# Kernel tuning notes

Measured on AMD Instinct MI355X. Metric: run time of the kernel, lower is better.

Reference implementation:

```python
import jax, jax.numpy as jnp
import numpy as np

N = 2048; C_IN = 2; H = 32; EMB = 16; OUT = 1; HORIZON = 12
B = 32; T = 16

def setup_inputs() -> dict:
    key = jax.random.key(0)
    ks = jax.random.split(key, 10)
    s = 0.05
    return {
        "x":  jax.random.normal(ks[0], (B, T, N, C_IN), dtype=jnp.float32),
        "E1": jax.random.normal(ks[1], (N, EMB), dtype=jnp.float32) * 0.1,
        "E2": jax.random.normal(ks[2], (N, EMB), dtype=jnp.float32) * 0.1,
        "Wx": jax.random.normal(ks[3], (C_IN, 4 * H), dtype=jnp.float32) * s,
        "bx": jnp.zeros((4 * H,), dtype=jnp.float32),
        "Wh": jax.random.normal(ks[4], (H, 4 * H), dtype=jnp.float32) * s,
        "bh": jnp.zeros((4 * H,), dtype=jnp.float32),
        "Wp": jax.random.normal(ks[5], (H, OUT * HORIZON), dtype=jnp.float32) * s,
        "bp": jnp.zeros((OUT * HORIZON,), dtype=jnp.float32),
    }

def reference(x, E1, E2, Wx, bx, Wh, bh, Wp, bp):
    Bb, Tt, Nn, _ = x.shape
    # adaptive adjacency: softmax(relu(E1 @ E2^T)) over last dim  [N,N]
    A = jax.nn.softmax(jax.nn.relu(E1 @ E2.T), axis=-1)

    def step(carry, xt):
        h, c = carry  # [B,N,H]
        # fused graph-conv gates: (A @ xt) Wx + (A @ h) Wh + biases -> [B,N,4H]
        gates = (jnp.einsum('ij,bjc->bic', A, xt) @ Wx + bx
                 + jnp.einsum('ij,bjh->bih', A, h) @ Wh + bh)
        i, f, o, g = jnp.split(gates, 4, axis=-1)
        i = jax.nn.sigmoid(i); f = jax.nn.sigmoid(f); o = jax.nn.sigmoid(o)
        g = jnp.tanh(g)
        c_t = f * c + i * g
        h_t = o * jnp.tanh(c_t)
        return (h_t, c_t), None

    h0 = jnp.zeros((Bb, Nn, H), dtype=x.dtype)
    c0 = jnp.zeros((Bb, Nn, H), dtype=x.dtype)
    (h_last, _), _ = jax.lax.scan(step, (h0, c0), jnp.transpose(x, (1, 0, 2, 3)))
    out = h_last @ Wp + bp                      # [B,N,horizon*out]
    out = out.reshape(Bb, Nn, HORIZON, OUT)
    return jnp.transpose(out, (0, 2, 1, 3))     # [B,horizon,N,out]
```

## Files before the change

kernel.cpp:

```cpp
#include <hip/hip_runtime.h>
#include <hip/hip_bf16.h>
#include <cstddef>
#include <cstdint>

#define NN 2048
#define CIN 2
#define HH 32
#define EMB 16
#define HOR 12
#define BB 32
#define TT 16
#define GC 128
#define XCOLS 1024
#define HCOLS 1024

#define ATILE_STRIDE 65536
#define BTILE_STRIDE 32768
#define LOPLANE 2097152

typedef __attribute__((ext_vector_type(8))) _Float16 f16x8;
typedef __attribute__((ext_vector_type(16))) float f32x16;

__device__ __forceinline__ void load_lds16(const void* g, void* l) {
    __builtin_amdgcn_global_load_lds(
        (const __attribute__((address_space(1))) void*)g,
        (__attribute__((address_space(3))) void*)l, 16, 0, 0);
}

__global__ __launch_bounds__(256) void adj_softmax(const float* __restrict__ E1,
                                                   const float* __restrict__ E2,
                                                   _Float16* __restrict__ A2) {
    const int i = blockIdx.x;
    __shared__ float red[256];
    float e1[EMB];
#pragma unroll
    for (int k = 0; k < EMB; ++k) e1[k] = E1[i * EMB + k];

    float s[8];
    float mx = -1e30f;
#pragma unroll
    for (int q = 0; q < 8; ++q) {
        const int j = q * 256 + threadIdx.x;
        float d = 0.f;
#pragma unroll
        for (int k = 0; k < EMB; ++k) d += e1[k] * E2[j * EMB + k];
        d = fmaxf(d, 0.0f);
        s[q] = d;
        mx = fmaxf(mx, d);
    }
    red[threadIdx.x] = mx;
    __syncthreads();
    for (int off = 128; off > 0; off >>= 1) {
        if (threadIdx.x < off) red[threadIdx.x] = fmaxf(red[threadIdx.x], red[threadIdx.x + off]);
        __syncthreads();
    }
    mx = red[0];
    __syncthreads();

    float sum = 0.f;
#pragma unroll
    for (int q = 0; q < 8; ++q) { s[q] = expf(s[q] - mx); sum += s[q]; }
    red[threadIdx.x] = sum;
    __syncthreads();
    for (int off = 128; off > 0; off >>= 1) {
        if (threadIdx.x < off) red[threadIdx.x] += red[threadIdx.x + off];
        __syncthreads();
    }
    const float inv = 1.0f / red[0];
#pragma unroll
    for (int q = 0; q < 8; ++q) {
        const int j  = q * 256 + threadIdx.x;
        const int tt = j >> 5, ko = (j >> 3) & 3, e = j & 7;
        A2[((size_t)(tt * 4 + ko) * 2048 + i) * 8 + e] = (_Float16)(s[q] * inv);
    }
}

__global__ __launch_bounds__(256) void transpose_x(const float* __restrict__ x,
                                                   _Float16* __restrict__ B2x) {
    const int idx = blockIdx.x * 256 + threadIdx.x;
    const int col = idx >> 11;
    const int j   = idx & (NN - 1);
    const int bt  = col >> 1;
    const int c   = col & 1;
    const float v = x[((size_t)bt * NN + j) * CIN + c];
    const _Float16 hi = (_Float16)v;
    const _Float16 lo = (_Float16)(v - (float)hi);
    const int tt = j >> 5, ko = (j >> 3) & 3, e = j & 7;
    const size_t base = ((size_t)(tt * 4 + ko) * 1024 + col) * 8 + e;
    B2x[base] = hi; B2x[base + LOPLANE] = lo;
}

template <int NPROD, int GATE>
__global__ __launch_bounds__(512, 2) void gemm_fused(const _Float16* __restrict__ A2,
                                                     const _Float16* __restrict__ B2,
                                                     float* __restrict__ Cout,
                                                     const float* __restrict__ AX,
                                                     const _Float16* __restrict__ W16,
                                                     const float* __restrict__ Wxr,
                                                     const float* __restrict__ bfold,
                                                     float* __restrict__ cst,
                                                     float* __restrict__ h32,
                                                     _Float16* __restrict__ hTout,
                                                     int t, int last) {
    constexpr int SUBS   = (NPROD == 1) ? 2 : 1;
    constexpr int NT     = 64 / SUBS;
    constexpr int SUBBUF = 4096 + NPROD * 8192;
    constexpr int BUF    = SUBS * SUBBUF;
    constexpr int NBUF   = (NPROD == 1) ? 4 : 6;
    constexpr int PCH    = 256 + NPROD * 512;
    constexpr int NG     = (SUBS * PCH) / 64;
    constexpr int GMAX   = 3;
    constexpr int STAGE_SZ = NBUF * BUF;
    constexpr int SMEMSZ = GATE ? (STAGE_SZ + 1024 + 512 + 2048) : STAGE_SZ;
    __shared__ __align__(16) char smem[SMEMSZ];

    const int tid  = threadIdx.x;
    const int w    = tid >> 6;
    const int lane = tid & 63;

    const int wg = blockIdx.x;
    const int x8 = wg & 7;
    const int s  = wg >> 3;
    const int mb = (x8 >> 1) * 8 + (s & 7);
    const int nb = (x8 & 1) * 4 + (s >> 3);
    const int m0 = mb * 64;
    const int n0 = nb * 128;

    float* wxr_s = nullptr; float* bfl_s = nullptr; float* axs = nullptr;
    if constexpr (GATE) {
        wxr_s = (float*)(smem + STAGE_SZ);
        bfl_s = (float*)(smem + STAGE_SZ + 1024);
        axs   = (float*)(smem + STAGE_SZ + 1536);
        const int b0c = nb * 4;
        if (tid < 64) *(float4*)&wxr_s[tid * 4] = *(const float4*)&Wxr[tid * 4];
        if (tid < 32) *(float4*)&bfl_s[tid * 4] = *(const float4*)&bfold[tid * 4];
        axs[tid] = AX[(size_t)(m0 + (tid & 63)) * XCOLS +
                      ((b0c + (tid >> 7)) * TT + t) * CIN + ((tid >> 6) & 1)];
    }

    const _Float16* gp[GMAX];
    int lbase[GMAX];
    int adv[GMAX];
    bool val[GMAX];
#pragma unroll
    for (int i = 0; i < GMAX; ++i) {
        const int g = w + 8 * i;
        val[i] = (g < NG);
        const int gg = val[i] ? g : 0;
        const int cid  = gg * 64 + lane;
        const int cid0 = gg * 64;
        const int su  = cid / PCH,  r  = cid  - su * PCH;
        const int su0 = cid0 / PCH, r0 = cid0 - su0 * PCH;
        if (r < 256) {
            gp[i]  = A2 + ((size_t)((su * 4 + (r >> 6)) * 2048) + m0 + (r & 63)) * 8;
            adv[i] = SUBS * ATILE_STRIDE;
        } else {
            const int r2 = r - 256;
            gp[i]  = B2 + (size_t)(r2 >> 9) * LOPLANE
                        + ((size_t)((su * 4 + ((r2 & 511) >> 7)) * 1024) + n0 + (r2 & 127)) * 8;
            adv[i] = SUBS * BTILE_STRIDE;
        }
        lbase[i] = su0 * SUBBUF + (r0 < 256 ? r0 * 16 : 4096 + (r0 - 256) * 16);
    }

    const int lrow = lane & 31, lg = lane >> 5;
    const int mi = w >> 2;
    const int gq = w & 3;
    const int wc = gq * 32;
    const int aoff0 = lg * 1024 + (mi * 32 + lrow) * 16;
    const int aoff1 = 2048 + lg * 1024 + (mi * 32 + lrow) * 16;
    const int boff0 = 4096 + lg * 2048 + (wc + lrow) * 16;
    const int boff1 = 4096 + 4096 + lg * 2048 + (wc + lrow) * 16;

    f32x16 acc0 = (f32x16)(0.0f), acc1 = (f32x16)(0.0f);

#define STAGE(BUFI) do {                                                       \
    char* lb = smem + (BUFI) * BUF;                                            \
    _Pragma("unroll")                                                          \
    for (int i = 0; i < GMAX; ++i) if (val[i]) {                               \
        load_lds16(gp[i], lb + lbase[i]);                                      \
        gp[i] += adv[i];                                                       \
    }                                                                          \
} while (0)

#define VMW(NHI, NLO) do {                                                     \
    if (w < 4) asm volatile("s_waitcnt vmcnt(" #NHI ")" ::: "memory");         \
    else       asm volatile("s_waitcnt vmcnt(" #NLO ")" ::: "memory");         \
} while (0)

#define BAR() do {                                                             \
    __builtin_amdgcn_s_barrier();                                              \
    asm volatile("" ::: "memory");                                             \
} while (0)

#define COMPUTE(BUFI) do {                                                     \
    const char* sb = smem + (BUFI) * BUF;                                      \
    _Pragma("unroll")                                                          \
    for (int su = 0; su < SUBS; ++su) {                                        \
        const char* st = sb + su * SUBBUF;                                     \
        f16x8 fa0 = *(const f16x8*)(st + aoff0);                               \
        f16x8 fa1 = *(const f16x8*)(st + aoff1);                               \
        f16x8 fb0 = *(const f16x8*)(st + boff0);                               \
        f16x8 fb1 = *(const f16x8*)(st + boff1);                               \
        acc0 = __builtin_amdgcn_mfma_f32_32x32x16_f16(fa0, fb0, acc0, 0, 0, 0);\
        acc1 = __builtin_amdgcn_mfma_f32_32x32x16_f16(fa1, fb1, acc1, 0, 0, 0);\
        if constexpr (NPROD == 2) {                                            \
            f16x8 fc0 = *(const f16x8*)(st + boff0 + 8192);                    \
            f16x8 fc1 = *(const f16x8*)(st + boff1 + 8192);                    \
            acc0 = __builtin_amdgcn_mfma_f32_32x32x16_f16(fa0, fc0, acc0, 0, 0, 0); \
            acc1 = __builtin_amdgcn_mfma_f32_32x32x16_f16(fa1, fc1, acc1, 0, 0, 0); \
        }                                                                      \
    }                                                                          \
} while (0)

    if constexpr (NPROD == 1) {
        STAGE(0);
        STAGE(1);
#pragma unroll 1
        for (int it = 0; it < NT - 2; ++it) {
            STAGE((it + 2) & 3);
            asm volatile("s_waitcnt vmcnt(6)" ::: "memory");
            BAR();
            COMPUTE(it & 3);
        }
        asm volatile("s_waitcnt vmcnt(3)" ::: "memory");
        BAR();
        COMPUTE((NT - 2) & 3);
        asm volatile("s_waitcnt vmcnt(0)" ::: "memory");
        BAR();
        COMPUTE((NT - 1) & 3);
    } else {
        STAGE(0);
        STAGE(1);
        STAGE(2);
        int bs = 3, bc = 0;
#pragma unroll 1
        for (int it = 0; it < NT - 3; ++it) {
            STAGE(bs);
            VMW(9, 6);
            BAR();
            COMPUTE(bc);
            bs = (bs == 5) ? 0 : bs + 1;
            bc = (bc == 5) ? 0 : bc + 1;
        }
        VMW(6, 4);
        BAR();
        COMPUTE(bc); bc = (bc == 5) ? 0 : bc + 1;
        VMW(3, 2);
        BAR();
        COMPUTE(bc); bc = (bc == 5) ? 0 : bc + 1;
        asm volatile("s_waitcnt vmcnt(0)" ::: "memory");
        BAR();
        COMPUTE(bc);
    }
#undef STAGE
#undef VMW
#undef BAR
#undef COMPUTE

    if constexpr (!GATE) {
        const int colg = n0 + wc + lrow;
#pragma unroll
        for (int r = 0; r < 16; ++r) {
            const int rp = (r & 3) + 8 * (r >> 2) + 4 * lg;
            Cout[(size_t)(m0 + mi * 32 + rp) * XCOLS + colg] = acc0[r] + acc1[r];
        }
    } else {
        f16x8 wbh0 = *(const f16x8*)(W16 + ((size_t)(0 * 4 + gq) * 64 + lane) * 8);
        f16x8 wbh1 = *(const f16x8*)(W16 + ((size_t)(1 * 4 + gq) * 64 + lane) * 8);
        f16x8 wbl0 = *(const f16x8*)(W16 + 8192 + ((size_t)(0 * 4 + gq) * 64 + lane) * 8);
        f16x8 wbl1 = *(const f16x8*)(W16 + 8192 + ((size_t)(1 * 4 + gq) * 64 + lane) * 8);

        _Float16* ahh = (_Float16*)smem;
        _Float16* ahl = (_Float16*)(smem + 17408);
        const int colw = wc + lrow;
#pragma unroll
        for (int r = 0; r < 16; ++r) {
            const int rp = (r & 3) + 8 * (r >> 2) + 4 * lg;
            const float v = acc0[r] + acc1[r];
            const _Float16 hi = (_Float16)v;
            ahh[(mi * 32 + rp) * 136 + colw] = hi;
            ahl[(mi * 32 + rp) * 136 + colw] = (_Float16)(v - (float)hi);
        }
        __syncthreads();

        f32x16 g0 = (f32x16)(0.0f), g1 = (f32x16)(0.0f);
        f32x16 g2 = (f32x16)(0.0f), g3 = (f32x16)(0.0f);
#define GATEB(ACC, b) do {                                                         \
    const int arow = (mi * 32 + lrow) * 136 + (b) * 32 + lg * 8;                   \
    f16x8 fh0 = *(const f16x8*)(ahh + arow);                                       \
    f16x8 fl0 = *(const f16x8*)(ahl + arow);                                       \
    f16x8 fh1 = *(const f16x8*)(ahh + arow + 16);                                  \
    f16x8 fl1 = *(const f16x8*)(ahl + arow + 16);                                  \
    ACC = __builtin_amdgcn_mfma_f32_32x32x16_f16(fh0, wbh0, ACC, 0, 0, 0);         \
    ACC = __builtin_amdgcn_mfma_f32_32x32x16_f16(fh0, wbl0, ACC, 0, 0, 0);         \
    ACC = __builtin_amdgcn_mfma_f32_32x32x16_f16(fl0, wbh0, ACC, 0, 0, 0);         \
    ACC = __builtin_amdgcn_mfma_f32_32x32x16_f16(fh1, wbh1, ACC, 0, 0, 0);         \
    ACC = __builtin_amdgcn_mfma_f32_32x32x16_f16(fh1, wbl1, ACC, 0, 0, 0);         \
    ACC = __builtin_amdgcn_mfma_f32_32x32x16_f16(fl1, wbh1, ACC, 0, 0, 0);         \
} while (0)
        GATEB(g0, 0); GATEB(g1, 1); GATEB(g2, 2); GATEB(g3, 3);
#undef GATEB

        float* gl = (float*)(smem + 34816);
        const int nl2 = tid & 63;
        const int hb  = (tid >> 6) * 4;
        const int b0c = nb * 4;
        const int nd  = m0 + nl2;
        const size_t ntbase = ((size_t)((nd >> 5) * 4 + ((nd >> 3) & 3)) * 1024) * 8 + (nd & 7);

#define POINT(ACC, bi) do {                                                        \
    _Pragma("unroll")                                                              \
    for (int r = 0; r < 16; ++r) {                                                 \
        const int rp = (r & 3) + 8 * (r >> 2) + 4 * lg;                            \
        gl[(mi * 32 + rp) * 132 + gq * 32 + lrow] = ACC[r];                        \
    }                                                                              \
    __syncthreads();                                                               \
    {                                                                              \
        const float ax0 = axs[(bi) * 128 + nl2];                                   \
        const float ax1 = axs[(bi) * 128 + 64 + nl2];                              \
        const int bb = b0c + (bi);                                                 \
        const size_t off = (size_t)nd * HCOLS + bb * HH + hb;                      \
        const float4 co = *(const float4*)(cst + off);                             \
        const float cold[4] = {co.x, co.y, co.z, co.w};                            \
        float cn[4], hn[4];                                                        \
        _Pragma("unroll")                                                          \
        for (int p = 0; p < 4; ++p) {                                              \
            const int hh = hb + p;                                                 \
            const float4 gt = *(const float4*)(gl + nl2 * 132 + hh * 4);           \
            const float a0 = gt.x + bfl_s[hh*4+0] + ax0*wxr_s[hh*4+0] + ax1*wxr_s[128+hh*4+0]; \
            const float a1 = gt.y + bfl_s[hh*4+1] + ax0*wxr_s[hh*4+1] + ax1*wxr_s[128+hh*4+1]; \
            const float a2 = gt.z + bfl_s[hh*4+2] + ax0*wxr_s[hh*4+2] + ax1*wxr_s[128+hh*4+2]; \
            const float a3 = gt.w + bfl_s[hh*4+3] + ax0*wxr_s[hh*4+3] + ax1*wxr_s[128+hh*4+3]; \
            const float i_ = 1.0f / (1.0f + expf(-a0));                            \
            const float f_ = 1.0f / (1.0f + expf(-a1));                            \
            const float o_ = 1.0f / (1.0f + expf(-a2));                            \
            const float g_ = tanhf(a3);                                            \
            const float ct = f_ * cold[p] + i_ * g_;                               \
            cn[p] = ct;                                                            \
            hn[p] = o_ * tanhf(ct);                                                \
        }                                                                          \
        *(float4*)(cst + off) = make_float4(cn[0], cn[1], cn[2], cn[3]);           \
        if (last) *(float4*)(h32 + off) = make_float4(hn[0], hn[1], hn[2], hn[3]); \
        _Pragma("unroll")                                                          \
        for (int p = 0; p < 4; ++p)                                                \
            hTout[ntbase + (size_t)(bb * HH + hb + p) * 8] = (_Float16)hn[p];      \
    }                                                                              \
    __syncthreads();                                                               \
} while (0)
        POINT(g0, 0); POINT(g1, 1); POINT(g2, 2); POINT(g3, 3);
#undef POINT
    }
}

__global__ __launch_bounds__(256) void prep_weights(const float* __restrict__ Wx,
                                                    const float* __restrict__ bx,
                                                    const float* __restrict__ Wh,
                                                    const float* __restrict__ bh,
                                                    _Float16* __restrict__ W16,
                                                    float* __restrict__ Wxr,
                                                    float* __restrict__ bfold) {
    const int tid = threadIdx.x;
#pragma unroll
    for (int r = 0; r < 32; ++r) {
        const int idx = r * 256 + tid;
        const int e  = idx & 7;
        const int ln = (idx >> 3) & 63;
        const int gq = (idx >> 9) & 3;
        const int kh = (idx >> 11) & 1;
        const int k  = kh * 16 + (ln >> 5) * 8 + e;
        const int ch = gq * 32 + (ln & 31);
        const float v = Wh[k * GC + (ch & 3) * HH + (ch >> 2)];
        const _Float16 hi = (_Float16)v;
        W16[idx] = hi;
        W16[8192 + idx] = (_Float16)(v - (float)hi);
    }
    {
        const int idx = tid;
        const int c = idx >> 7, rem = idx & 127;
        const int h = rem >> 2, g = rem & 3;
        Wxr[idx] = Wx[c * GC + g * HH + h];
    }
    if (tid < 128) {
        const int h = tid >> 2, g = tid & 3;
        bfold[tid] = bx[g * HH + h] + bh[g * HH + h];
    }
}

__global__ __launch_bounds__(256) void gate_update(const float* __restrict__ AX,
                                                   const float* __restrict__ Wxr,
                                                   const float* __restrict__ bfold,
                                                   float* __restrict__ c,
                                                   float* __restrict__ h32,
                                                   _Float16* __restrict__ hT) {
    const int n0 = blockIdx.x * 64;
    const int b0 = blockIdx.y * 4;
    const int tid = threadIdx.x;
    __shared__ float wxr[256];
    __shared__ float bfl[128];
    __shared__ float axs[2][64];

    if (tid < 64)  *(float4*)&wxr[tid * 4] = *(const float4*)&Wxr[tid * 4];
    if (tid < 32)  *(float4*)&bfl[tid * 4] = *(const float4*)&bfold[tid * 4];

    const int nl = tid & 63;
    const int hq = tid >> 6;

    const int nd = n0 + nl;
    const size_t ntbase = ((size_t)((nd >> 5) * 4 + ((nd >> 3) & 3)) * 1024) * 8 + (nd & 7);

#pragma unroll 1
    for (int bi = 0; bi < 4; ++bi) {
        const int b = b0 + bi;
        if (bi) __syncthreads();
        if (tid < 128) {
            const int which = tid >> 6, nls = tid & 63;
            axs[which][nls] = AX[(size_t)(n0 + nls) * XCOLS + (b * TT + 0) * CIN + which];
        }
        __syncthreads();

        const float ax0 = axs[0][nl], ax1 = axs[1][nl];
        float cn[8], hn[8];
#pragma unroll
        for (int u = 0; u < 8; ++u) {
            const int h = hq * 8 + u;
            float a0 = bfl[h * 4 + 0] + ax0 * wxr[h * 4 + 0] + ax1 * wxr[128 + h * 4 + 0];
            float a1 = bfl[h * 4 + 1] + ax0 * wxr[h * 4 + 1] + ax1 * wxr[128 + h * 4 + 1];
            float a2 = bfl[h * 4 + 2] + ax0 * wxr[h * 4 + 2] + ax1 * wxr[128 + h * 4 + 2];
            float a3 = bfl[h * 4 + 3] + ax0 * wxr[h * 4 + 3] + ax1 * wxr[128 + h * 4 + 3];
            const float i_ = 1.0f / (1.0f + expf(-a0));
            const float f_ = 1.0f / (1.0f + expf(-a1));
            const float o_ = 1.0f / (1.0f + expf(-a2));
            const float g_ = tanhf(a3);
            const float ct = i_ * g_;
            (void)f_;
            cn[u] = ct;
            hn[u] = o_ * tanhf(ct);
        }
        const size_t off = (size_t)nd * HCOLS + b * HH + hq * 8;
        *(float4*)(c + off)       = make_float4(cn[0], cn[1], cn[2], cn[3]);
        *(float4*)(c + off + 4)   = make_float4(cn[4], cn[5], cn[6], cn[7]);
        *(float4*)(h32 + off)     = make_float4(hn[0], hn[1], hn[2], hn[3]);
        *(float4*)(h32 + off + 4) = make_float4(hn[4], hn[5], hn[6], hn[7]);
#pragma unroll
        for (int u = 0; u < 8; ++u)
            hT[ntbase + (size_t)(b * HH + hq * 8 + u) * 8] = (_Float16)hn[u];
    }
}

__global__ __launch_bounds__(256) void head_kernel(const float* __restrict__ h,
                                                   const float* __restrict__ Wp,
                                                   const float* __restrict__ bp,
                                                   float* __restrict__ out) {
    const int idx = blockIdx.x * 256 + threadIdx.x;
    const int b = idx >> 11;
    const int n = idx & (NN - 1);
    float hv[HH];
    const float* hp = h + (size_t)n * HCOLS + b * HH;
#pragma unroll
    for (int k = 0; k < HH; ++k) hv[k] = hp[k];
#pragma unroll
    for (int th = 0; th < HOR; ++th) {
        float acc = bp[th];
#pragma unroll
        for (int k = 0; k < HH; ++k) acc += hv[k] * Wp[k * HOR + th];
        out[((size_t)b * HOR + th) * NN + n] = acc;
    }
}

extern "C" void kernel_launch(void* const* d_in, const int* in_sizes, int n_in,
                              void* d_out, int out_size, void* d_ws, size_t ws_size,
                              hipStream_t stream) {
    const float* x  = (const float*)d_in[0];
    const float* E1 = (const float*)d_in[1];
    const float* E2 = (const float*)d_in[2];
    const float* Wx = (const float*)d_in[3];
    const float* bx = (const float*)d_in[4];
    const float* Wh = (const float*)d_in[5];
    const float* bh = (const float*)d_in[6];
    const float* Wp = (const float*)d_in[7];
    const float* bp = (const float*)d_in[8];

    char* ws = (char*)d_ws;
    _Float16* A2  = (_Float16*)(ws);
    _Float16* B2x = (_Float16*)(ws + ( 8ull << 20));
    _Float16* hT0 = (_Float16*)(ws + (16ull << 20));
    _Float16* hT1 = (_Float16*)(ws + (20ull << 20));
    float* AX   = (float*)(ws + (24ull << 20));
    float* cst  = (float*)(ws + (32ull << 20));
    float* h32  = (float*)(ws + (40ull << 20));
    float* Wxr  = (float*)(ws + (48ull << 20) + 65536);
    float* bfold= (float*)(ws + (48ull << 20) + 131072);
    _Float16* W16 = (_Float16*)(ws + (48ull << 20) + 262144);
    _Float16* hTb[2] = {hT0, hT1};

    adj_softmax<<<NN, 256, 0, stream>>>(E1, E2, A2);
    transpose_x<<<(XCOLS * NN) / 256, 256, 0, stream>>>(x, B2x);
    prep_weights<<<1, 256, 0, stream>>>(Wx, bx, Wh, bh, W16, Wxr, bfold);

    gemm_fused<2, 0><<<256, 512, 0, stream>>>(A2, B2x, AX, nullptr, nullptr, nullptr,
                                              nullptr, nullptr, nullptr, nullptr, 0, 0);

    gate_update<<<dim3(NN / 64, BB / 4), 256, 0, stream>>>(AX, Wxr, bfold,
                                                           cst, h32, hTb[0]);
    for (int t = 1; t < TT; ++t) {
        gemm_fused<1, 1><<<256, 512, 0, stream>>>(A2, hTb[(t + 1) & 1], nullptr, AX,
                                                  W16, Wxr, bfold, cst, h32,
                                                  hTb[t & 1], t, t == TT - 1 ? 1 : 0);
    }

    head_kernel<<<(BB * NN) / 256, 256, 0, stream>>>(h32, Wp, bp, (float*)d_out);
}
```

Measured before the change: 558.8 us.

## Double K-step per stage and switch to 3-buffer single-barrier pipeline

Doubles the number of K sub-tiles loaded per pipeline stage (SUBS 2→4 / 1→2), halving the loop iteration count. Replaces the 4/6-deep buffer rings with a 3-buffer ring where the next stage is issued after the barrier, so one barrier per iteration protects both reads and overwrites. This removes per-lane validity predicates and uneven wave wait counts, and adds a barrier before the gate epilogue reuses shared memory. The trade-off is larger stages with shallower prefetch depth, and LDS use per block changes, which may affect the two-blocks-per-CU occupancy.

After: 576.2 us. +3.1%, slower.

```diff
diff --git a/kernel.cpp b/kernel.cpp
--- a/kernel.cpp
+++ b/kernel.cpp
@@ -102,15 +102,14 @@
                                                      float* __restrict__ h32,
                                                      _Float16* __restrict__ hTout,
                                                      int t, int last) {
-    constexpr int SUBS   = (NPROD == 1) ? 2 : 1;
+    constexpr int SUBS   = (NPROD == 1) ? 4 : 2;
     constexpr int NT     = 64 / SUBS;
     constexpr int SUBBUF = 4096 + NPROD * 8192;
     constexpr int BUF    = SUBS * SUBBUF;
-    constexpr int NBUF   = (NPROD == 1) ? 4 : 6;
     constexpr int PCH    = 256 + NPROD * 512;
     constexpr int NG     = (SUBS * PCH) / 64;
-    constexpr int GMAX   = 3;
-    constexpr int STAGE_SZ = NBUF * BUF;
+    constexpr int GMAX   = NG / 8;
+    constexpr int STAGE_SZ = 3 * BUF;
     constexpr int SMEMSZ = GATE ? (STAGE_SZ + 1024 + 512 + 2048) : STAGE_SZ;
     __shared__ __align__(16) char smem[SMEMSZ];
 
@@ -141,14 +140,11 @@
     const _Float16* gp[GMAX];
     int lbase[GMAX];
     int adv[GMAX];
-    bool val[GMAX];
 #pragma unroll
     for (int i = 0; i < GMAX; ++i) {
         const int g = w + 8 * i;
-        val[i] = (g < NG);
-        const int gg = val[i] ? g : 0;
-        const int cid  = gg * 64 + lane;
-        const int cid0 = gg * 64;
+        const int cid  = g * 64 + lane;
+        const int cid0 = g * 64;
         const int su  = cid / PCH,  r  = cid  - su * PCH;
         const int su0 = cid0 / PCH, r0 = cid0 - su0 * PCH;
         if (r < 256) {
@@ -177,15 +173,10 @@
 #define STAGE(BUFI) do {                                                       \
     char* lb = smem + (BUFI) * BUF;                                            \
     _Pragma("unroll")                                                          \
-    for (int i = 0; i < GMAX; ++i) if (val[i]) {                               \
+    for (int i = 0; i < GMAX; ++i) {                                           \
         load_lds16(gp[i], lb + lbase[i]);                                      \
         gp[i] += adv[i];                                                       \
     }                                                                          \
-} while (0)
-
-#define VMW(NHI, NLO) do {                                                     \
-    if (w < 4) asm volatile("s_waitcnt vmcnt(" #NHI ")" ::: "memory");         \
-    else       asm volatile("s_waitcnt vmcnt(" #NLO ")" ::: "memory");         \
 } while (0)
 
 #define BAR() do {                                                             \
@@ -213,48 +204,29 @@
     }                                                                          \
 } while (0)
 
-    if constexpr (NPROD == 1) {
-        STAGE(0);
-        STAGE(1);
+    STAGE(0);
+    STAGE(1);
+    {
+        int bs = 2, bc = 0;
 #pragma unroll 1
-        for (int it = 0; it < NT - 2; ++it) {
-            STAGE((it + 2) & 3);
-            asm volatile("s_waitcnt vmcnt(6)" ::: "memory");
+        for (int it = 0; it < NT - 1; ++it) {
+            if constexpr (NPROD == 1)
+                asm volatile("s_waitcnt vmcnt(6)" ::: "memory");
+            else
+                asm volatile("s_waitcnt vmcnt(5)" ::: "memory");
             BAR();
-            COMPUTE(it & 3);
-        }
-        asm volatile("s_waitcnt vmcnt(3)" ::: "memory");
-        BAR();
-        COMPUTE((NT - 2) & 3);
-        asm volatile("s_waitcnt vmcnt(0)" ::: "memory");
-        BAR();
-        COMPUTE((NT - 1) & 3);
-    } else {
-        STAGE(0);
-        STAGE(1);
-        STAGE(2);
-        int bs = 3, bc = 0;
-#pragma unroll 1
-        for (int it = 0; it < NT - 3; ++it) {
-            STAGE(bs);
-            VMW(9, 6);
-            BAR();
+            if (it < NT - 2) {
+                STAGE(bs);
+                bs = (bs == 2) ? 0 : bs + 1;
+            }
             COMPUTE(bc);
-            bs = (bs == 5) ? 0 : bs + 1;
-            bc = (bc == 5) ? 0 : bc + 1;
-        }
-        VMW(6, 4);
-        BAR();
-        COMPUTE(bc); bc = (bc == 5) ? 0 : bc + 1;
-        VMW(3, 2);
-        BAR();
-        COMPUTE(bc); bc = (bc == 5) ? 0 : bc + 1;
+            bc = (bc == 2) ? 0 : bc + 1;
+        }
         asm volatile("s_waitcnt vmcnt(0)" ::: "memory");
         BAR();
         COMPUTE(bc);
     }
 #undef STAGE
-#undef VMW
 #undef BAR
 #undef COMPUTE
 
@@ -270,6 +242,8 @@
         f16x8 wbh1 = *(const f16x8*)(W16 + ((size_t)(1 * 4 + gq) * 64 + lane) * 8);
         f16x8 wbl0 = *(const f16x8*)(W16 + 8192 + ((size_t)(0 * 4 + gq) * 64 + lane) * 8);
         f16x8 wbl1 = *(const f16x8*)(W16 + 8192 + ((size_t)(1 * 4 + gq) * 64 + lane) * 8);
+
+        __syncthreads();
 
         _Float16* ahh = (_Float16*)smem;
         _Float16* ahl = (_Float16*)(smem + 17408);
```
